# Optimization experiments

Measured on AMD Instinct MI355X. Metric: run time of the kernel, lower is better.

The kernel has to match this reference:

```python
import jax, jax.numpy as jnp
import numpy as np

DIM = 768
HEADS = 12
HD = DIM // HEADS
SCALE = float(np.sqrt(HD))  # sqrt(dim // num_heads)


def layernorm(x, g, b, eps=1e-5):
    m = jnp.mean(x, axis=-1, keepdims=True)
    v = jnp.var(x, axis=-1, keepdims=True)
    return (x - m) * jax.lax.rsqrt(v + eps) * g + b


def dwconv(x, w, b, pad):
    # x: [B,C,H,W], w: [C,1,kh,kw] depthwise
    y = jax.lax.conv_general_dilated(
        x, w, window_strides=(1, 1), padding=[(pad, pad), (pad, pad)],
        feature_group_count=x.shape[1], dimension_numbers=('NCHW', 'OIHW', 'NCHW'))
    return y + b[None, :, None, None]


def mha(xq, xkv, wq, bq, wk, bk, wv, bv, wo, bo):
    # per-head Linears batched over heads; wq/wk/wv: [H, C, hd], biases [H, hd]
    B, N, C = xq.shape
    q = jnp.einsum('bnc,hcd->bhnd', xq, wq) + bq[None, :, None, :]
    k = jnp.einsum('bnc,hcd->bhnd', xkv, wk) + bk[None, :, None, :]
    v = jnp.einsum('bnc,hcd->bhnd', xkv, wv) + bv[None, :, None, :]
    z = jax.nn.sigmoid(jnp.einsum('bhnd,bhmd->bhnm', q, k) / SCALE)  # sigmoid, not softmax
    o = jnp.einsum('bhnm,bhmd->bhnd', z, v)
    o = o.transpose(0, 2, 1, 3).reshape(B, N, C)  # concat heads along feature dim
    return o @ wo + bo


def reference(decoder, wq1, bq1, wk1, bk1, wv1, bv1, wo1, bo1,
              wq2, bq2, wk2, bk2, wv2, bv2, wo2, bo2,
              alphas1, alphas2, peg_w, peg_b,
              ln1_g, ln1_b, ln2_g, ln2_b,
              cn_dw_w, cn_dw_b, cn_ln_g, cn_ln_b,
              cn_w1, cn_b1, cn_w2, cn_b2, cn_scale, cn_alphas):
    B, C, H, W = decoder.shape
    x = decoder.transpose(0, 2, 3, 1).reshape(B, H * W, C)  # [B,N,C]
    # block 1: alpha * x + MHA(x,x,x)
    x = alphas1 * x + mha(x, x, wq1, bq1, wk1, bk1, wv1, bv1, wo1, bo1)
    # PEG: depthwise 3x3 conv (replaces x, no residual in source)
    x4 = x.reshape(B, H, W, C).transpose(0, 3, 1, 2)
    x4 = dwconv(x4, peg_w, peg_b, pad=1)
    x = x4.transpose(0, 2, 3, 1).reshape(B, H * W, C)
    x = layernorm(x, ln1_g, ln1_b)
    # block 2 (encoder is None -> self-attention)
    x = alphas2 * x + mha(x, x, wq2, bq2, wk2, bk2, wv2, bv2, wo2, bo2)
    x = layernorm(x, ln2_g, ln2_b)
    x4 = x.reshape(B, H, W, C).transpose(0, 3, 1, 2)  # [B,C,H,W]
    # CNBlock head: dwconv7x7 -> LN -> Linear(4d) -> GELU -> Linear(d), layer_scale + alpha residual
    y = dwconv(x4, cn_dw_w, cn_dw_b, pad=3)
    y = y.transpose(0, 2, 3, 1)  # [B,H,W,C]
    y = layernorm(y, cn_ln_g, cn_ln_b)
    y = jax.nn.gelu(y @ cn_w1 + cn_b1, approximate=False)
    y = y @ cn_w2 + cn_b2
    y = y.transpose(0, 3, 1, 2)  # [B,C,H,W]
    out = cn_scale[None, :, None, None] * y + x4 * cn_alphas[None, :, None, None]
    return out


def setup_inputs() -> dict:
    key = jax.random.key(0)
    ks = iter(jax.random.split(key, 40))
    def n(shape, s=0.02):
        return jax.random.normal(next(ks), shape, dtype=jnp.float32) * s
    d = {}
    d['decoder'] = jax.random.normal(next(ks), (8, DIM, 32, 32), dtype=jnp.float32)
    for i in (1, 2):
        d[f'wq{i}'] = n((HEADS, DIM, HD)); d[f'bq{i}'] = n((HEADS, HD), 1e-6)
        d[f'wk{i}'] = n((HEADS, DIM, HD)); d[f'bk{i}'] = n((HEADS, HD), 1e-6)
        d[f'wv{i}'] = n((HEADS, DIM, HD)); d[f'bv{i}'] = n((HEADS, HD), 1e-6)
        d[f'wo{i}'] = n((DIM, DIM)); d[f'bo{i}'] = n((DIM,), 1e-6)
    d['alphas1'] = jnp.ones((DIM,), jnp.float32)
    d['alphas2'] = jnp.ones((DIM,), jnp.float32)
    d['peg_w'] = n((DIM, 1, 3, 3), 0.1); d['peg_b'] = n((DIM,), 1e-6)
    d['ln1_g'] = jnp.ones((DIM,), jnp.float32); d['ln1_b'] = jnp.zeros((DIM,), jnp.float32)
    d['ln2_g'] = jnp.ones((DIM,), jnp.float32); d['ln2_b'] = jnp.zeros((DIM,), jnp.float32)
    d['cn_dw_w'] = n((DIM, 1, 7, 7), 0.1); d['cn_dw_b'] = n((DIM,), 0.02)
    d['cn_ln_g'] = jnp.ones((DIM,), jnp.float32); d['cn_ln_b'] = jnp.zeros((DIM,), jnp.float32)
    d['cn_w1'] = n((DIM, 4 * DIM)); d['cn_b1'] = n((4 * DIM,), 0.02)
    d['cn_w2'] = n((4 * DIM, DIM)); d['cn_b2'] = n((DIM,), 0.02)
    d['cn_scale'] = jnp.full((DIM,), 1e-6, jnp.float32)
    d['cn_alphas'] = jnp.ones((DIM,), jnp.float32)
    return d
```

## Files before the change

### kernel.cpp

```cpp
#include <hip/hip_runtime.h>
#include <math.h>

#define BATCH 8
#define CDIM 768
#define NTOK 1024
#define NH 12
#define HDIM 64

typedef __attribute__((ext_vector_type(8))) short bf16x8;
typedef __attribute__((ext_vector_type(4))) float f32x4;

__device__ inline short f2bf(float f) {
    union { float f; unsigned u; } v; v.f = f;
    unsigned r = (v.u + 0x7FFF + ((v.u >> 16) & 1)) >> 16;
    return (short)r;
}

__device__ inline unsigned pack2bf(float lo, float hi) {
    return (unsigned)(unsigned short)f2bf(lo) | ((unsigned)(unsigned short)f2bf(hi) << 16);
}

__device__ inline void async_copy16(const short* g, short* l) {
    __builtin_amdgcn_global_load_lds(
        (const __attribute__((address_space(1))) void*)g,
        (__attribute__((address_space(3))) void*)l, 16, 0, 0);
}

__global__ __launch_bounds__(256) void k_prep(
    const float* __restrict__ wq1, const float* __restrict__ wk1, const float* __restrict__ wv1,
    const float* __restrict__ wq2, const float* __restrict__ wk2, const float* __restrict__ wv2,
    const float* __restrict__ wo1, const float* __restrict__ wo2,
    const float* __restrict__ cnw1, const float* __restrict__ cnw2,
    const float* __restrict__ bq1, const float* __restrict__ bk1, const float* __restrict__ bv1,
    const float* __restrict__ bq2, const float* __restrict__ bk2, const float* __restrict__ bv2,
    const float* __restrict__ dec,
    short* __restrict__ Wqkv1, short* __restrict__ Wqkv2,
    short* __restrict__ WoT1, short* __restrict__ WoT2,
    short* __restrict__ W1T, short* __restrict__ W2T,
    float* __restrict__ bqkv1, float* __restrict__ bqkv2,
    float* __restrict__ A0, short* __restrict__ Xb) {
    __shared__ float sh[64 * 65];
    int bid = blockIdx.x;
    int t = threadIdx.x;
    if (bid < 864) {
        int bx = bid % 12, z = bid / 12;
        int set = z / 36, rem = z % 36, sect = rem / 12, hh = rem % 12;
        const float* srcs[6] = {wq1, wk1, wv1, wq2, wk2, wv2};
        const float* src = srcs[set * 3 + sect] + (size_t)hh * 768 * 64;
        short* dst = (set ? Wqkv2 : Wqkv1) + ((size_t)sect * 768 + hh * 64) * 768;
        int k0 = bx * 64;
#pragma unroll
        for (int p = 0; p < 16; ++p) {
            int gid = t + p * 256;
            int r = gid >> 6, c = gid & 63;
            sh[r * 65 + c] = src[(size_t)(k0 + r) * 64 + c];
        }
        __syncthreads();
#pragma unroll
        for (int p = 0; p < 16; ++p) {
            int gid = t + p * 256;
            int d = gid >> 6, kk = gid & 63;
            dst[(size_t)d * 768 + k0 + kk] = f2bf(sh[kk * 65 + d]);
        }
    } else if (bid < 6624) {
        int r = bid - 864;
        const float* src; short* dst; int R, C, bx, by;
        if (r < 576)       { src = wo1;  dst = WoT1; R = 768;  C = 768;  bx = r % 24; by = r / 24; }
        else if (r < 1152) { int s = r - 576;  src = wo2;  dst = WoT2; R = 768;  C = 768;  bx = s % 24; by = s / 24; }
        else if (r < 3456) { int s = r - 1152; src = cnw1; dst = W1T;  R = 768;  C = 3072; bx = s % 96; by = s / 96; }
        else               { int s = r - 3456; src = cnw2; dst = W2T;  R = 3072; C = 768;  bx = s % 24; by = s / 24; }
        int c0 = bx * 32, r0 = by * 32, tx = t & 31, ty = t >> 5;
#pragma unroll
        for (int p = 0; p < 4; ++p)
            sh[(ty + p * 8) * 33 + tx] = src[(size_t)(r0 + ty + p * 8) * C + c0 + tx];
        __syncthreads();
#pragma unroll
        for (int p = 0; p < 4; ++p)
            dst[(size_t)(c0 + ty + p * 8) * R + r0 + tx] = f2bf(sh[tx * 33 + ty + p * 8]);
    } else if (bid < 6642) {
        int tid = (bid - 6624) * 256 + t;
        if (tid < 4608) {
            int set = tid / 2304, n = tid % 2304;
            int sect = n / 768, rem = n % 768;
            const float* srcs[6] = {bq1, bk1, bv1, bq2, bk2, bv2};
            float v = srcs[set * 3 + sect][rem];
            (set ? bqkv2 : bqkv1)[n] = v;
        }
    } else {
        int r = bid - 6642;
        int bx = r % 32, by = (r / 32) % 24, bz = r / 768;
        int n0 = bx * 32, c0 = by * 32, tx = t & 31, ty = t >> 5;
#pragma unroll
        for (int p = 0; p < 4; ++p) {
            int c = c0 + ty + p * 8;
            sh[(ty + p * 8) * 33 + tx] = dec[((size_t)bz * CDIM + c) * NTOK + n0 + tx];
        }
        __syncthreads();
#pragma unroll
        for (int p = 0; p < 4; ++p) {
            int n = n0 + ty + p * 8;
            float val = sh[tx * 33 + ty + p * 8];
            size_t idx = ((size_t)bz * NTOK + n) * CDIM + c0 + tx;
            A0[idx] = val;
            Xb[idx] = f2bf(val);
        }
    }
}

#define GM_FINAL 0
#define GM_PROJ  1
#define GM_GELU  2
#define GM_QKV   3
#define QKVSEC ((size_t)BATCH * NH * NTOK * HDIM)

template<int MODE, int BN>
__global__ __launch_bounds__(256) void k_gemm_mfma(
    const short* __restrict__ A, const short* __restrict__ Bt,
    const float* __restrict__ bias, const float* __restrict__ resid,
    const float* __restrict__ rscale, const float* __restrict__ alph,
    float* __restrict__ outF, short* __restrict__ outB, int M, int N, int K) {
    constexpr int NT = BN / 32;
    constexpr int BP = BN / 64;
    constexpr int STAGE = 2 * 128 * 32 + 2 * BN * 32;
    constexpr int FINALS = (MODE == GM_FINAL) ? 64 * 132 * 2 : 0;
    constexpr int SMEM = STAGE > FINALS ? STAGE : FINALS;
    __shared__ short smem[SMEM];
    short* As = smem;
    short* Bs = smem + 2 * 128 * 32;
    int t = threadIdx.x;
    int w = t >> 6, lane = t & 63, l15 = lane & 15, quad = lane >> 4;
    int r0 = blockIdx.x * 128, n0 = blockIdx.y * BN;
    int wr = (w >> 1) * 64, wc = (w & 1) * (BN / 2);
    f32x4 acc[4][NT];
#pragma unroll
    for (int i = 0; i < 4; ++i)
#pragma unroll
        for (int j = 0; j < NT; ++j) acc[i][j] = (f32x4){0.f, 0.f, 0.f, 0.f};
    int sr = t >> 2, sc = (t & 3) * 8;
    const short* Ag = A + (size_t)(r0 + sr) * K + sc;
    const short* Bg = Bt + (size_t)(n0 + sr) * K + sc;
    short* AsW = As + w * 512;
    short* BsW = Bs + w * 512;
#pragma unroll
    for (int p = 0; p < 2; ++p)
        async_copy16(Ag + (size_t)p * 64 * K, AsW + p * 2048);
#pragma unroll
    for (int p = 0; p < BP; ++p)
        async_copy16(Bg + (size_t)p * 64 * K, BsW + p * 2048);
    int st = 0;
    for (int k0 = 0; k0 < K; k0 += 32, st ^= 1) {
        __syncthreads();
        if (k0 + 32 < K) {
            int nst = st ^ 1;
#pragma unroll
            for (int p = 0; p < 2; ++p)
                async_copy16(Ag + k0 + 32 + (size_t)p * 64 * K,
                             AsW + nst * 4096 + p * 2048);
#pragma unroll
            for (int p = 0; p < BP; ++p)
                async_copy16(Bg + k0 + 32 + (size_t)p * 64 * K,
                             BsW + nst * (BN * 32) + p * 2048);
        }
        bf16x8 af[4], bf[NT];
#pragma unroll
        for (int i = 0; i < 4; ++i)
            af[i] = *(const bf16x8*)&As[st * 4096 + (wr + i * 16 + l15) * 32 + quad * 8];
#pragma unroll
        for (int j = 0; j < NT; ++j)
            bf[j] = *(const bf16x8*)&Bs[st * (BN * 32) + (wc + j * 16 + l15) * 32 + quad * 8];
#pragma unroll
        for (int i = 0; i < 4; ++i)
#pragma unroll
            for (int j = 0; j < NT; ++j)
                acc[i][j] = __builtin_amdgcn_mfma_f32_16x16x32_bf16(af[i], bf[j], acc[i][j], 0, 0, 0);
    }
    if (MODE == GM_FINAL) {
        __syncthreads();
        float* T = (float*)smem;
#pragma unroll
        for (int i = 0; i < 4; ++i)
#pragma unroll
            for (int j = 0; j < NT; ++j)
#pragma unroll
                for (int rr = 0; rr < 4; ++rr) {
                    int rl = wr + i * 16 + quad * 4 + rr;
                    int cl = wc + j * 16 + l15;
                    int row = r0 + rl, col = n0 + cl;
                    float val = acc[i][j][rr] + bias[col];
                    val = rscale[col] * val + alph[col] * resid[(size_t)row * N + col];
                    T[cl * 132 + rl] = val;
                }
        __syncthreads();
        int c = t >> 2, qo = (t & 3) * 32;
        int b = r0 >> 10, tokbase = r0 & 1023;
        float* obase = outF + ((size_t)(b * 768 + n0 + c)) * 1024 + tokbase + qo;
#pragma unroll
        for (int ii = 0; ii < 8; ++ii)
            *(float4*)&obase[ii * 4] = *(float4*)&T[c * 132 + qo + ii * 4];
        return;
    }
#pragma unroll
    for (int i = 0; i < 4; ++i)
#pragma unroll
        for (int j = 0; j < NT; ++j)
#pragma unroll
            for (int rr = 0; rr < 4; ++rr) {
                int row = r0 + wr + i * 16 + quad * 4 + rr;
                int col = n0 + wc + j * 16 + l15;
                float val = acc[i][j][rr] + bias[col];
                if (MODE == GM_PROJ) {
                    val += rscale[col] * resid[(size_t)row * N + col];
                    outF[(size_t)row * N + col] = val;
                } else if (MODE == GM_GELU) {
                    float u = val * (1.0f + 0.044715f * val * val);
                    float zz = __builtin_amdgcn_rcpf(
                        1.0f + __builtin_amdgcn_exp2f(-2.3022082f * u));
                    outB[(size_t)row * N + col] = f2bf(val * zz);
                } else {
                    int sect = col / 768, rem = col - sect * 768;
                    int hh = rem >> 6, d = rem & 63;
                    int bb = row >> 10, tok = row & 1023;
                    outB[(size_t)sect * QKVSEC +
                         (((size_t)bb * NH + hh) * NTOK + tok) * HDIM + d] = f2bf(val);
                }
            }
}

__global__ __launch_bounds__(256, 3) void k_attn_mfma(
    const short* __restrict__ q, const short* __restrict__ k,
    const short* __restrict__ v, short* __restrict__ o) {
    __shared__ short Ks[2][64 * 64];
    __shared__ short Vt[2][64][72];
    __shared__ short Ps[128][72];
    int t = threadIdx.x;
    int w = t >> 6, lane = t & 63, l15 = lane & 15, quad = lane >> 4;
    int flat = blockIdx.x + (blockIdx.y << 3) + blockIdx.z * 96;
    int xcd = flat & 7, slot = flat >> 3;
    int qb = slot & 7, grp = xcd * 12 + (slot >> 3);
    int h = grp % 12, b = grp / 12;
    int q0 = qb * 128;
    size_t base = ((size_t)(b * NH + h)) * NTOK * HDIM;
    const short* qp = q + base;
    const short* kp = k + base;
    const short* vp = v + base;

    bf16x8 qf[2][2];
#pragma unroll
    for (int nq = 0; nq < 2; ++nq)
#pragma unroll
        for (int kc = 0; kc < 2; ++kc)
            qf[nq][kc] = *(const bf16x8*)&qp[(size_t)(q0 + w * 32 + nq * 16 + l15) * HDIM + kc * 32 + quad * 8];

    int r8 = lane >> 3;
    const short* kg = kp + r8 * HDIM + (((lane & 7) ^ r8) << 3);
    int vtok = t & 63, vd0 = (t >> 6) * 8;

    f32x4 oacc[4][2];
#pragma unroll
    for (int dt = 0; dt < 4; ++dt)
#pragma unroll
        for (int nq = 0; nq < 2; ++nq) oacc[dt][nq] = (f32x4){0.f, 0.f, 0.f, 0.f};

#pragma unroll
    for (int p = 0; p < 2; ++p)
        async_copy16(kg + (size_t)(p * 32 + w * 8) * HDIM, &Ks[0][(p * 32 + w * 8) * 64]);
    {
        bf16x8 v0 = *(const bf16x8*)&vp[(size_t)vtok * HDIM + vd0];
        bf16x8 v1 = *(const bf16x8*)&vp[(size_t)vtok * HDIM + vd0 + 32];
#pragma unroll
        for (int j = 0; j < 8; ++j) {
            Vt[0][vd0 + j][vtok] = v0[j];
            Vt[0][vd0 + 32 + j][vtok] = v1[j];
        }
    }

    short* prow0 = &Ps[w * 32 + l15][0];
    short* prow1 = &Ps[w * 32 + 16 + l15][0];

    for (int kt = 0; kt < 16; ++kt) {
        int cur = kt & 1, nxt = cur ^ 1;
        __syncthreads();
        bf16x8 vv0, vv1;
        if (kt < 15) {
            const short* kgn = kg + (size_t)((kt + 1) * 64) * HDIM;
#pragma unroll
            for (int p = 0; p < 2; ++p)
                async_copy16(kgn + (size_t)(p * 32 + w * 8) * HDIM, &Ks[nxt][(p * 32 + w * 8) * 64]);
            vv0 = *(const bf16x8*)&vp[((size_t)(kt + 1) * 64 + vtok) * HDIM + vd0];
            vv1 = *(const bf16x8*)&vp[((size_t)(kt + 1) * 64 + vtok) * HDIM + vd0 + 32];
        }
        f32x4 sacc[4][2];
#pragma unroll
        for (int mk = 0; mk < 4; ++mk)
#pragma unroll
            for (int nq = 0; nq < 2; ++nq) sacc[mk][nq] = (f32x4){0.f, 0.f, 0.f, 0.f};
        __builtin_amdgcn_s_setprio(1);
#pragma unroll
        for (int mk = 0; mk < 4; ++mk)
#pragma unroll
            for (int kc = 0; kc < 2; ++kc) {
                bf16x8 kf = *(const bf16x8*)&Ks[cur][(mk * 16 + l15) * 64 + (((kc * 4 + quad) ^ (l15 & 7)) << 3)];
#pragma unroll
                for (int nq = 0; nq < 2; ++nq)
                    sacc[mk][nq] = __builtin_amdgcn_mfma_f32_16x16x32_bf16(kf, qf[nq][kc], sacc[mk][nq], 0, 0, 0);
            }
        __builtin_amdgcn_s_setprio(0);
#pragma unroll
        for (int mk = 0; mk < 4; ++mk)
#pragma unroll
            for (int nq = 0; nq < 2; ++nq) {
                float z[4];
#pragma unroll
                for (int rr = 0; rr < 4; ++rr)
                    z[rr] = __builtin_amdgcn_rcpf(
                        1.0f + __builtin_amdgcn_exp2f(sacc[mk][nq][rr] * -0.18033688011112042f));
                unsigned* pw = (unsigned*)((nq ? prow1 : prow0) + mk * 16 + quad * 4);
                pw[0] = pack2bf(z[0], z[1]);
                pw[1] = pack2bf(z[2], z[3]);
            }
        if (kt < 15) {
#pragma unroll
            for (int j = 0; j < 8; ++j) {
                Vt[nxt][vd0 + j][vtok] = vv0[j];
                Vt[nxt][vd0 + 32 + j][vtok] = vv1[j];
            }
        }
        asm volatile("s_waitcnt lgkmcnt(0)" ::: "memory");
        __builtin_amdgcn_sched_barrier(0);
        bf16x8 pf[2][2];
#pragma unroll
        for (int kc = 0; kc < 2; ++kc)
#pragma unroll
            for (int nq = 0; nq < 2; ++nq)
                pf[kc][nq] = *(const bf16x8*)((nq ? prow1 : prow0) + kc * 32 + quad * 8);
        __builtin_amdgcn_s_setprio(1);
#pragma unroll
        for (int dt = 0; dt < 4; ++dt)
#pragma unroll
            for (int kc = 0; kc < 2; ++kc) {
                bf16x8 vf = *(const bf16x8*)&Vt[cur][dt * 16 + l15][kc * 32 + quad * 8];
#pragma unroll
                for (int nq = 0; nq < 2; ++nq)
                    oacc[dt][nq] = __builtin_amdgcn_mfma_f32_16x16x32_bf16(vf, pf[kc][nq], oacc[dt][nq], 0, 0, 0);
            }
        __builtin_amdgcn_s_setprio(0);
    }
#pragma unroll
    for (int dt = 0; dt < 4; ++dt)
#pragma unroll
        for (int nq = 0; nq < 2; ++nq) {
            int tok = q0 + w * 32 + nq * 16 + l15;
            int c = h * 64 + dt * 16 + quad * 4;
            unsigned* op = (unsigned*)&o[((size_t)b * NTOK + tok) * CDIM + c];
            op[0] = pack2bf(oacc[dt][nq][0], oacc[dt][nq][1]);
            op[1] = pack2bf(oacc[dt][nq][2], oacc[dt][nq][3]);
        }
}

template<int K>
__global__ __launch_bounds__(256) void k_dwconv_t(
    const float* __restrict__ in, const float* __restrict__ w,
    const float* __restrict__ bias, float* __restrict__ out) {
    constexpr int PAD = K / 2;
    constexpr int KK = K * K;
    int t = threadIdx.x;
    int c = blockIdx.y * 64 + (t & 63);
    int j = blockIdx.x * 4 + (t >> 6);
    int b = blockIdx.z;
    float wr[KK];
#pragma unroll
    for (int qq = 0; qq < KK; ++qq) wr[qq] = w[(size_t)c * KK + qq];
    float bsv = bias[c];
    const float* base = in + (size_t)b * NTOK * CDIM + c;
    float win[K][K];
#pragma unroll
    for (int s = 1; s < K; ++s) {
        int ii = s - 1 - PAD;
#pragma unroll
        for (int qq = 0; qq < K; ++qq) {
            int jj = j - PAD + qq;
            win[s][qq] = (ii >= 0 && jj >= 0 && jj < 32)
                         ? base[(size_t)(ii * 32 + jj) * CDIM] : 0.0f;
        }
    }
#pragma unroll
    for (int i = 0; i < 32; ++i) {
#pragma unroll
        for (int r = 0; r < K - 1; ++r)
#pragma unroll
            for (int qq = 0; qq < K; ++qq) win[r][qq] = win[r + 1][qq];
        int ii = i + PAD;
#pragma unroll
        for (int qq = 0; qq < K; ++qq) {
            int jj = j - PAD + qq;
            win[K - 1][qq] = (ii < 32 && jj >= 0 && jj < 32)
                             ? base[(size_t)(ii * 32 + jj) * CDIM] : 0.0f;
        }
        float acc = bsv;
#pragma unroll
        for (int r = 0; r < K; ++r)
#pragma unroll
            for (int qq = 0; qq < K; ++qq)
                acc = fmaf(win[r][qq], wr[r * K + qq], acc);
        out[((size_t)b * NTOK + i * 32 + j) * CDIM + c] = acc;
    }
}

__global__ __launch_bounds__(256) void k_ln(
    const float* __restrict__ in, const float* __restrict__ g,
    const float* __restrict__ b, float* __restrict__ outF, short* __restrict__ outB) {
    int row = blockIdx.x;
    const float* xr = in + (size_t)row * CDIM;
    int t = threadIdx.x;
    float x0 = xr[t], x1 = xr[t + 256], x2 = xr[t + 512];
    float s = x0 + x1 + x2;
    float sq = x0 * x0 + x1 * x1 + x2 * x2;
#pragma unroll
    for (int off = 32; off > 0; off >>= 1) {
        s += __shfl_down(s, off);
        sq += __shfl_down(sq, off);
    }
    __shared__ float ws[4], wq2[4];
    int wid = t >> 6, lane = t & 63;
    if (lane == 0) { ws[wid] = s; wq2[wid] = sq; }
    __syncthreads();
    if (t == 0) {
        float S = ws[0] + ws[1] + ws[2] + ws[3];
        float Q = wq2[0] + wq2[1] + wq2[2] + wq2[3];
        float m = S * (1.0f / CDIM);
        float var = Q * (1.0f / CDIM) - m * m;
        ws[0] = m;
        wq2[0] = rsqrtf(var + 1e-5f);
    }
    __syncthreads();
    float m = ws[0], inv = wq2[0];
    float y0 = (x0 - m) * inv * g[t] + b[t];
    float y1 = (x1 - m) * inv * g[t + 256] + b[t + 256];
    float y2 = (x2 - m) * inv * g[t + 512] + b[t + 512];
    if (outF) {
        float* orow = outF + (size_t)row * CDIM;
        orow[t] = y0; orow[t + 256] = y1; orow[t + 512] = y2;
    }
    if (outB) {
        short* orow = outB + (size_t)row * CDIM;
        orow[t] = f2bf(y0); orow[t + 256] = f2bf(y1); orow[t + 512] = f2bf(y2);
    }
}

extern "C" void kernel_launch(void* const* d_in, const int* in_sizes, int n_in,
                              void* d_out, int out_size, void* d_ws, size_t ws_size,
                              hipStream_t stream) {
    const float* dec = (const float*)d_in[0];
    const float* wq1 = (const float*)d_in[1]; const float* bq1 = (const float*)d_in[2];
    const float* wk1 = (const float*)d_in[3]; const float* bk1 = (const float*)d_in[4];
    const float* wv1 = (const float*)d_in[5]; const float* bv1 = (const float*)d_in[6];
    const float* wo1 = (const float*)d_in[7]; const float* bo1 = (const float*)d_in[8];
    const float* wq2 = (const float*)d_in[9]; const float* bq2 = (const float*)d_in[10];
    const float* wk2 = (const float*)d_in[11]; const float* bk2 = (const float*)d_in[12];
    const float* wv2 = (const float*)d_in[13]; const float* bv2 = (const float*)d_in[14];
    const float* wo2 = (const float*)d_in[15]; const float* bo2 = (const float*)d_in[16];
    const float* alphas1 = (const float*)d_in[17];
    const float* alphas2 = (const float*)d_in[18];
    const float* peg_w = (const float*)d_in[19]; const float* peg_b = (const float*)d_in[20];
    const float* ln1_g = (const float*)d_in[21]; const float* ln1_b = (const float*)d_in[22];
    const float* ln2_g = (const float*)d_in[23]; const float* ln2_b = (const float*)d_in[24];
    const float* cn_dw_w = (const float*)d_in[25]; const float* cn_dw_b = (const float*)d_in[26];
    const float* cn_ln_g = (const float*)d_in[27]; const float* cn_ln_b = (const float*)d_in[28];
    const float* cn_w1 = (const float*)d_in[29]; const float* cn_b1 = (const float*)d_in[30];
    const float* cn_w2 = (const float*)d_in[31]; const float* cn_b2 = (const float*)d_in[32];
    const float* cn_scale = (const float*)d_in[33]; const float* cn_alphas = (const float*)d_in[34];
    float* out = (float*)d_out;

    const size_t S = (size_t)BATCH * NTOK * CDIM;
    float* A0 = (float*)d_ws;
    float* A1 = A0 + S;
    short* Xb  = (short*)(A1 + S);
    short* QKV = Xb + S;
    short* Ob  = QKV + 3 * S;
    short* Hb  = Ob + S;
    short* Wqkv1 = Hb + 2 * S;
    short* Wqkv2 = Wqkv1 + 2304 * 768;
    short* WoT1  = Wqkv2 + 2304 * 768;
    short* WoT2  = WoT1 + 768 * 768;
    short* W1T   = WoT2 + 768 * 768;
    short* W2T   = W1T + (size_t)3072 * 768;
    float* bqkv1 = (float*)(W2T + (size_t)768 * 3072);
    float* bqkv2 = bqkv1 + 2304;
    short* Hfull = QKV + 2 * S;

    dim3 dwgrid(8, 12, 8);

    k_prep<<<dim3(12786), 256, 0, stream>>>(
        wq1, wk1, wv1, wq2, wk2, wv2, wo1, wo2, cn_w1, cn_w2,
        bq1, bk1, bv1, bq2, bk2, bv2, dec,
        Wqkv1, Wqkv2, WoT1, WoT2, W1T, W2T, bqkv1, bqkv2, A0, Xb);

    k_gemm_mfma<GM_QKV, 128><<<dim3(64, 18), 256, 0, stream>>>(
        Xb, Wqkv1, bqkv1, nullptr, nullptr, nullptr, nullptr, QKV, 8192, 2304, 768);
    k_attn_mfma<<<dim3(8, 12, 8), 256, 0, stream>>>(QKV, QKV + S, QKV + 2 * S, Ob);
    k_gemm_mfma<GM_PROJ, 64><<<dim3(64, 12), 256, 0, stream>>>(
        Ob, WoT1, bo1, A0, alphas1, nullptr, A1, nullptr, 8192, 768, 768);
    k_dwconv_t<3><<<dwgrid, 256, 0, stream>>>(A1, peg_w, peg_b, A0);
    k_ln<<<8192, 256, 0, stream>>>(A0, ln1_g, ln1_b, A1, Xb);

    k_gemm_mfma<GM_QKV, 128><<<dim3(64, 18), 256, 0, stream>>>(
        Xb, Wqkv2, bqkv2, nullptr, nullptr, nullptr, nullptr, QKV, 8192, 2304, 768);
    k_attn_mfma<<<dim3(8, 12, 8), 256, 0, stream>>>(QKV, QKV + S, QKV + 2 * S, Ob);
    k_gemm_mfma<GM_PROJ, 64><<<dim3(64, 12), 256, 0, stream>>>(
        Ob, WoT2, bo2, A1, alphas2, nullptr, A0, nullptr, 8192, 768, 768);
    k_ln<<<8192, 256, 0, stream>>>(A0, ln2_g, ln2_b, A1, nullptr);

    k_dwconv_t<7><<<dwgrid, 256, 0, stream>>>(A1, cn_dw_w, cn_dw_b, A0);
    k_ln<<<8192, 256, 0, stream>>>(A0, cn_ln_g, cn_ln_b, nullptr, Xb);
    k_gemm_mfma<GM_GELU, 128><<<dim3(64, 24), 256, 0, stream>>>(
        Xb, W1T, cn_b1, nullptr, nullptr, nullptr, nullptr, Hfull, 8192, 3072, 768);
    k_gemm_mfma<GM_FINAL, 64><<<dim3(64, 12), 256, 0, stream>>>(
        Hfull, W2T, cn_b2, A1, cn_scale, cn_alphas, out, nullptr, 8192, 768, 3072);
}
```

Before: 578.6 us.

## Store QKV row-major and swizzle GEMM LDS tiles to avoid bank conflicts

The QKV GEMM now writes its output as a plain row-major [tokens, 2304] matrix instead of scattering into per-head [B,H,N,64] sections, and the attention kernel reads Q/K/V with a 2304-element row stride. Separately, the GEMM LDS tile layout gets an XOR swizzle on the 16-byte chunk index, applied both to the async global-to-LDS copies and to the fragment reads, to reduce LDS bank conflicts. The epilogue stores become contiguous, but attention loads now stride across wider rows, which may lower their locality.

```diff
diff --git a/kernel.cpp b/kernel.cpp
--- a/kernel.cpp
+++ b/kernel.cpp
@@ -6,6 +6,7 @@
 #define NTOK 1024
 #define NH 12
 #define HDIM 64
+#define QKVN 2304
 
 typedef __attribute__((ext_vector_type(8))) short bf16x8;
 typedef __attribute__((ext_vector_type(4))) float f32x4;
@@ -110,8 +111,7 @@
 #define GM_FINAL 0
 #define GM_PROJ  1
 #define GM_GELU  2
-#define GM_QKV   3
-#define QKVSEC ((size_t)BATCH * NH * NTOK * HDIM)
+#define GM_BF16  3
 
 template<int MODE, int BN>
 __global__ __launch_bounds__(256) void k_gemm_mfma(
@@ -136,11 +136,12 @@
     for (int i = 0; i < 4; ++i)
 #pragma unroll
         for (int j = 0; j < NT; ++j) acc[i][j] = (f32x4){0.f, 0.f, 0.f, 0.f};
-    int sr = t >> 2, sc = (t & 3) * 8;
+    int sr = t >> 2, sc = ((t & 3) ^ ((sr >> 1) & 3)) * 8;
     const short* Ag = A + (size_t)(r0 + sr) * K + sc;
     const short* Bg = Bt + (size_t)(n0 + sr) * K + sc;
     short* AsW = As + w * 512;
     short* BsW = Bs + w * 512;
+    int rsw = ((quad ^ ((l15 >> 1) & 3)) << 3);
 #pragma unroll
     for (int p = 0; p < 2; ++p)
         async_copy16(Ag + (size_t)p * 64 * K, AsW + p * 2048);
@@ -164,10 +165,10 @@
         bf16x8 af[4], bf[NT];
 #pragma unroll
         for (int i = 0; i < 4; ++i)
-            af[i] = *(const bf16x8*)&As[st * 4096 + (wr + i * 16 + l15) * 32 + quad * 8];
+            af[i] = *(const bf16x8*)&As[st * 4096 + (wr + i * 16 + l15) * 32 + rsw];
 #pragma unroll
         for (int j = 0; j < NT; ++j)
-            bf[j] = *(const bf16x8*)&Bs[st * (BN * 32) + (wc + j * 16 + l15) * 32 + quad * 8];
+            bf[j] = *(const bf16x8*)&Bs[st * (BN * 32) + (wc + j * 16 + l15) * 32 + rsw];
 #pragma unroll
         for (int i = 0; i < 4; ++i)
 #pragma unroll
@@ -217,11 +218,7 @@
                         1.0f + __builtin_amdgcn_exp2f(-2.3022082f * u));
                     outB[(size_t)row * N + col] = f2bf(val * zz);
                 } else {
-                    int sect = col / 768, rem = col - sect * 768;
-                    int hh = rem >> 6, d = rem & 63;
-                    int bb = row >> 10, tok = row & 1023;
-                    outB[(size_t)sect * QKVSEC +
-                         (((size_t)bb * NH + hh) * NTOK + tok) * HDIM + d] = f2bf(val);
+                    outB[(size_t)row * N + col] = f2bf(val);
                 }
             }
 }
@@ -239,7 +236,7 @@
     int qb = slot & 7, grp = xcd * 12 + (slot >> 3);
     int h = grp % 12, b = grp / 12;
     int q0 = qb * 128;
-    size_t base = ((size_t)(b * NH + h)) * NTOK * HDIM;
+    size_t base = ((size_t)b * NTOK) * QKVN + h * 64;
     const short* qp = q + base;
     const short* kp = k + base;
     const short* vp = v + base;
@@ -249,10 +246,10 @@
     for (int nq = 0; nq < 2; ++nq)
 #pragma unroll
         for (int kc = 0; kc < 2; ++kc)
-            qf[nq][kc] = *(const bf16x8*)&qp[(size_t)(q0 + w * 32 + nq * 16 + l15) * HDIM + kc * 32 + quad * 8];
+            qf[nq][kc] = *(const bf16x8*)&qp[(size_t)(q0 + w * 32 + nq * 16 + l15) * QKVN + kc * 32 + quad * 8];
 
     int r8 = lane >> 3;
-    const short* kg = kp + r8 * HDIM + (((lane & 7) ^ r8) << 3);
+    const short* kg = kp + (size_t)r8 * QKVN + (((lane & 7) ^ r8) << 3);
     int vtok = t & 63, vd0 = (t >> 6) * 8;
 
     f32x4 oacc[4][2];
@@ -263,10 +260,10 @@
 
 #pragma unroll
     for (int p = 0; p < 2; ++p)
-        async_copy16(kg + (size_t)(p * 32 + w * 8) * HDIM, &Ks[0][(p * 32 + w * 8) * 64]);
+        async_copy16(kg + (size_t)(p * 32 + w * 8) * QKVN, &Ks[0][(p * 32 + w * 8) * 64]);
     {
-        bf16x8 v0 = *(const bf16x8*)&vp[(size_t)vtok * HDIM + vd0];
-        bf16x8 v1 = *(const bf16x8*)&vp[(size_t)vtok * HDIM + vd0 + 32];
+        bf16x8 v0 = *(const bf16x8*)&vp[(size_t)vtok * QKVN + vd0];
+        bf16x8 v1 = *(const bf16x8*)&vp[(size_t)vtok * QKVN + vd0 + 32];
 #pragma unroll
         for (int j = 0; j < 8; ++j) {
             Vt[0][vd0 + j][vtok] = v0[j];
@@ -282,12 +279,12 @@
         __syncthreads();
         bf16x8 vv0, vv1;
         if (kt < 15) {
-            const short* kgn = kg + (size_t)((kt + 1) * 64) * HDIM;
+            const short* kgn = kg + (size_t)((kt + 1) * 64) * QKVN;
 #pragma unroll
             for (int p = 0; p < 2; ++p)
-                async_copy16(kgn + (size_t)(p * 32 + w * 8) * HDIM, &Ks[nxt][(p * 32 + w * 8) * 64]);
-            vv0 = *(const bf16x8*)&vp[((size_t)(kt + 1) * 64 + vtok) * HDIM + vd0];
-            vv1 = *(const bf16x8*)&vp[((size_t)(kt + 1) * 64 + vtok) * HDIM + vd0 + 32];
+                async_copy16(kgn + (size_t)(p * 32 + w * 8) * QKVN, &Ks[nxt][(p * 32 + w * 8) * 64]);
+            vv0 = *(const bf16x8*)&vp[((size_t)((kt + 1) * 64 + vtok)) * QKVN + vd0];
+            vv1 = *(const bf16x8*)&vp[((size_t)((kt + 1) * 64 + vtok)) * QKVN + vd0 + 32];
         }
         f32x4 sacc[4][2];
 #pragma unroll
@@ -495,17 +492,17 @@
         bq1, bk1, bv1, bq2, bk2, bv2, dec,
         Wqkv1, Wqkv2, WoT1, WoT2, W1T, W2T, bqkv1, bqkv2, A0, Xb);
 
-    k_gemm_mfma<GM_QKV, 128><<<dim3(64, 18), 256, 0, stream>>>(
+    k_gemm_mfma<GM_BF16, 128><<<dim3(64, 18), 256, 0, stream>>>(
         Xb, Wqkv1, bqkv1, nullptr, nullptr, nullptr, nullptr, QKV, 8192, 2304, 768);
-    k_attn_mfma<<<dim3(8, 12, 8), 256, 0, stream>>>(QKV, QKV + S, QKV + 2 * S, Ob);
+    k_attn_mfma<<<dim3(8, 12, 8), 256, 0, stream>>>(QKV, QKV + 768, QKV + 1536, Ob);
     k_gemm_mfma<GM_PROJ, 64><<<dim3(64, 12), 256, 0, stream>>>(
         Ob, WoT1, bo1, A0, alphas1, nullptr, A1, nullptr, 8192, 768, 768);
     k_dwconv_t<3><<<dwgrid, 256, 0, stream>>>(A1, peg_w, peg_b, A0);
     k_ln<<<8192, 256, 0, stream>>>(A0, ln1_g, ln1_b, A1, Xb);
 
-    k_gemm_mfma<GM_QKV, 128><<<dim3(64, 18), 256, 0, stream>>>(
+    k_gemm_mfma<GM_BF16, 128><<<dim3(64, 18), 256, 0, stream>>>(
         Xb, Wqkv2, bqkv2, nullptr, nullptr, nullptr, nullptr, QKV, 8192, 2304, 768);
-    k_attn_mfma<<<dim3(8, 12, 8), 256, 0, stream>>>(QKV, QKV + S, QKV + 2 * S, Ob);
+    k_attn_mfma<<<dim3(8, 12, 8), 256, 0, stream>>>(QKV, QKV + 768, QKV + 1536, Ob);
     k_gemm_mfma<GM_PROJ, 64><<<dim3(64, 12), 256, 0, stream>>>(
         Ob, WoT2, bo2, A1, alphas2, nullptr, A0, nullptr, 8192, 768, 768);
     k_ln<<<8192, 256, 0, stream>>>(A0, ln2_g, ln2_b, A1, nullptr);
```

New measurement: 565.9 us, median of 2. 1.02x faster.
